# Kernel tuning notes

Measured on AMD Instinct MI355X. Metric: run time of the kernel, lower is better.

Reference implementation:

```python
import jax, jax.numpy as jnp
import numpy as np

B, S, HID, NH = 8, 1024, 768, 12
HD = HID // NH

def _linear_params(key, din, dout):
    kw, kb = jax.random.split(key)
    lim = 1.0 / np.sqrt(din)
    W = jax.random.uniform(kw, (din, dout), minval=-lim, maxval=lim, dtype=jnp.float32)
    b = jax.random.uniform(kb, (dout,), minval=-lim, maxval=lim, dtype=jnp.float32)
    return W, b

def setup_inputs() -> dict:
    key = jax.random.key(0)
    ks = jax.random.split(key, 10)
    query = jax.random.normal(ks[0], (B, S, HID), dtype=jnp.float32)
    key_t = jax.random.normal(ks[1], (B, S, HID), dtype=jnp.float32)
    value = jax.random.normal(ks[2], (B, S, HID), dtype=jnp.float32)
    mask = jax.random.randint(ks[3], (B, 1, 1, S), 0, 2, dtype=jnp.int32)
    Wq, bq = _linear_params(ks[4], HID, HID)
    Wk, bk = _linear_params(ks[5], HID, HID)
    Wv, bv = _linear_params(ks[6], HID, HID)
    Wo, bo = _linear_params(ks[7], HID, HID)
    W1, b1 = _linear_params(ks[8], 2 * HID, HID)
    W2, b2 = _linear_params(ks[9], 2 * HID, HID)
    return dict(query=query, key=key_t, value=value, mask=mask,
                Wq=Wq, bq=bq, Wk=Wk, bk=bk, Wv=Wv, bv=bv,
                Wo=Wo, bo=bo, W1=W1, b1=b1, W2=W2, b2=b2)

def reference(query, key, value, mask, Wq, bq, Wk, bk, Wv, bv, Wo, bo, W1, b1, W2, b2):
    scale = np.sqrt(HD).astype(np.float32)
    # project and split heads: [B,S,HID] -> [B,NH,S,HD]
    def heads(x, W, b):
        return (x @ W + b).reshape(B, S, NH, HD).transpose(0, 2, 1, 3)
    Q = heads(query, Wq, bq)
    K = heads(key, Wk, bk)
    V = heads(value, Wv, bv)
    energy = jnp.einsum('bhqd,bhkd->bhqk', Q, K) / scale  # [B,NH,S,S]
    energy = jnp.where(mask == 0, jnp.float32(-1e10), energy)
    attention = jax.nn.softmax(energy, axis=-1)
    x = jnp.einsum('bhqk,bhkd->bhqd', attention, V)
    x = x.transpose(0, 2, 1, 3).reshape(B, S, HID)
    x = x @ Wo + bo
    x = jnp.concatenate([x, query], axis=2)  # [B,S,2*HID]
    x1 = jax.nn.sigmoid(x @ W1 + b1)
    x2 = x @ W2 + b2
    return (x1 * x2, attention)
```

## Files before the change

### kernel.cpp

```cpp
#include <hip/hip_runtime.h>
#include <hip/hip_bf16.h>

#define Bn   8
#define Sn   1024
#define HIDn 768
#define NHn  12
#define HDn  64
#define MROWS (Bn * Sn)
#define OUT0  ((size_t)MROWS * HIDn)

typedef __attribute__((ext_vector_type(8))) short short8;
typedef __attribute__((ext_vector_type(4))) float f32x4;

__device__ __forceinline__ float bf2f(unsigned short u) {
    union { unsigned int i; float f; } v;
    v.i = ((unsigned int)u) << 16;
    return v.f;
}
__device__ __forceinline__ unsigned short f2bf(float f) {
    __hip_bfloat16 h = __float2bfloat16(f);
    return *reinterpret_cast<unsigned short*>(&h);
}

template <typename T> struct IsFP32              { static constexpr bool v = false; };
template <>           struct IsFP32<float>       { static constexpr bool v = true;  };

__device__ __forceinline__ float ld1f(const unsigned short* p) { return bf2f(*p); }
__device__ __forceinline__ float ld1f(const float* p)          { return *p; }

__device__ __forceinline__ void load8s(const unsigned short* p, short8& h, short8& l) {
    h = *(const short8*)p;
    #pragma unroll
    for (int t = 0; t < 8; ++t) l[t] = 0;
}
__device__ __forceinline__ void load8s(const float* p, short8& h, short8& l) {
    float4 a = *(const float4*)p;
    float4 b = *(const float4*)(p + 4);
    float f[8] = {a.x, a.y, a.z, a.w, b.x, b.y, b.z, b.w};
    #pragma unroll
    for (int t = 0; t < 8; ++t) {
        unsigned short hu = f2bf(f[t]);
        h[t] = (short)hu;
        l[t] = (short)f2bf(f[t] - bf2f(hu));
    }
}
__device__ __forceinline__ void load8k(const unsigned short* p, int stride, short8& h, short8& l) {
    #pragma unroll
    for (int t = 0; t < 8; ++t) { h[t] = (short)p[(size_t)t * stride]; l[t] = 0; }
}
__device__ __forceinline__ void load8k(const float* p, int stride, short8& h, short8& l) {
    #pragma unroll
    for (int t = 0; t < 8; ++t) {
        float f = p[(size_t)t * stride];
        unsigned short hu = f2bf(f);
        h[t] = (short)hu;
        l[t] = (short)f2bf(f - bf2f(hu));
    }
}

__global__ void probe_kernel(const unsigned short* __restrict__ q, int* __restrict__ flag) {
    __shared__ int cnt;
    if (threadIdx.x == 0) cnt = 0;
    __syncthreads();
    int ins = 0;
    for (int i = threadIdx.x; i < 4096; i += 256) {
        unsigned short u = q[2 * i];
        int e = (u >> 7) & 0xFF;
        float v = bf2f(u);
        if (e == 0xFF || fabsf(v) > 1e4f) ins++;
    }
    atomicAdd(&cnt, ins);
    __syncthreads();
    if (threadIdx.x == 0) *flag = (cnt > 400) ? 1 : 0;
}

template <typename TA, typename TA2, typename TW>
__launch_bounds__(256, 2)
__global__ void gemm_mfma(const TA*  __restrict__ A,
                          const TA2* __restrict__ A2,
                          int Ksplit, int K,
                          const TW* __restrict__ W,
                          const TW* __restrict__ bias,
                          const unsigned short* __restrict__ gate,
                          void* __restrict__ Cv, int c_fp32,
                          const int* __restrict__ flag, int mymode)
{
    if (*flag != mymode) return;

    constexpr bool AFP  = IsFP32<TA>::v;
    constexpr bool A2FP = IsFP32<TA2>::v;
    constexpr bool WFP  = IsFP32<TW>::v;

    __shared__ __align__(16) unsigned short Ash[128][40];
    __shared__ __align__(16) unsigned short Asl[128][40];
    __shared__ __align__(16) unsigned short Bth[64][40];
    __shared__ __align__(16) unsigned short Btl[64][40];

    const int tid  = threadIdx.x;
    const int lane = tid & 63;
    const int wid  = tid >> 6;
    const int wr   = wid >> 1;
    const int wc   = wid & 1;
    const int l15  = lane & 15;
    const int g    = lane >> 4;
    const int n0   = blockIdx.x * 64;
    const int m0   = blockIdx.y * 128;

    f32x4 acc[4][2];
    #pragma unroll
    for (int mi = 0; mi < 4; ++mi)
        #pragma unroll
        for (int ni = 0; ni < 2; ++ni)
            acc[mi][ni] = (f32x4){0.f, 0.f, 0.f, 0.f};

    for (int k0 = 0; k0 < K; k0 += 32) {
        const bool fromA = (k0 < Ksplit);
        const bool allo  = fromA ? AFP : A2FP;

        #pragma unroll
        for (int t = 0; t < 2; ++t) {
            const int idx = t * 256 + tid;
            const int row = idx >> 2;
            const int c8  = (idx & 3) * 8;
            short8 h, l;
            if (fromA) load8s(A  + (size_t)(m0 + row) * HIDn + k0 + c8, h, l);
            else       load8s(A2 + (size_t)(m0 + row) * HIDn + (k0 - Ksplit) + c8, h, l);
            *(short8*)&Ash[row][c8] = h;
            if (allo) *(short8*)&Asl[row][c8] = l;
        }
        {
            const int nn = tid >> 2;
            const int kg = (tid & 3) * 8;
            short8 h, l;
            load8k(W + (size_t)(k0 + kg) * HIDn + n0 + nn, HIDn, h, l);
            *(short8*)&Bth[nn][kg] = h;
            if (WFP) *(short8*)&Btl[nn][kg] = l;
        }
        __syncthreads();

        short8 ah[4], bh[2], al[4], bl[2];
        #pragma unroll
        for (int mi = 0; mi < 4; ++mi)
            ah[mi] = *(const short8*)&Ash[wr * 64 + mi * 16 + l15][g * 8];
        #pragma unroll
        for (int ni = 0; ni < 2; ++ni)
            bh[ni] = *(const short8*)&Bth[wc * 32 + ni * 16 + l15][g * 8];
        if (allo) {
            #pragma unroll
            for (int mi = 0; mi < 4; ++mi)
                al[mi] = *(const short8*)&Asl[wr * 64 + mi * 16 + l15][g * 8];
        }
        if (WFP) {
            #pragma unroll
            for (int ni = 0; ni < 2; ++ni)
                bl[ni] = *(const short8*)&Btl[wc * 32 + ni * 16 + l15][g * 8];
        }

        #pragma unroll
        for (int mi = 0; mi < 4; ++mi)
            #pragma unroll
            for (int ni = 0; ni < 2; ++ni)
                acc[mi][ni] = __builtin_amdgcn_mfma_f32_16x16x32_bf16(ah[mi], bh[ni], acc[mi][ni], 0, 0, 0);
        if (WFP) {
            #pragma unroll
            for (int mi = 0; mi < 4; ++mi)
                #pragma unroll
                for (int ni = 0; ni < 2; ++ni)
                    acc[mi][ni] = __builtin_amdgcn_mfma_f32_16x16x32_bf16(ah[mi], bl[ni], acc[mi][ni], 0, 0, 0);
        }
        if (allo) {
            #pragma unroll
            for (int mi = 0; mi < 4; ++mi)
                #pragma unroll
                for (int ni = 0; ni < 2; ++ni)
                    acc[mi][ni] = __builtin_amdgcn_mfma_f32_16x16x32_bf16(al[mi], bh[ni], acc[mi][ni], 0, 0, 0);
        }
        __syncthreads();
    }

    #pragma unroll
    for (int mi = 0; mi < 4; ++mi) {
        #pragma unroll
        for (int ni = 0; ni < 2; ++ni) {
            const int col = n0 + wc * 32 + ni * 16 + l15;
            const float bv = ld1f(bias + col);
            #pragma unroll
            for (int r = 0; r < 4; ++r) {
                const int row = m0 + wr * 64 + mi * 16 + g * 4 + r;
                float v = acc[mi][ni][r] + bv;
                if (gate) {
                    float gt = bf2f(gate[(size_t)row * HIDn + col]);
                    v = v / (1.f + expf(-gt));
                }
                const size_t idx = (size_t)row * HIDn + col;
                if (c_fp32) ((float*)Cv)[idx] = v;
                else        ((unsigned short*)Cv)[idx] = f2bf(v);
            }
        }
    }
}

#define QB 64
#define KT 128
#define KSTRIDE 72
#define VSTRIDE 136

__launch_bounds__(256, 2)
__global__ void attn_mfma_kernel(const unsigned short* __restrict__ Q,
                                 const unsigned short* __restrict__ Kb,
                                 const unsigned short* __restrict__ V,
                                 const int* __restrict__ mask,
                                 void* __restrict__ dout,
                                 unsigned short* __restrict__ xout,
                                 const int* __restrict__ flag)
{
    __shared__ __align__(16) unsigned short Qs[QB][KSTRIDE];
    __shared__ __align__(16) unsigned short Ks[KT][KSTRIDE];
    __shared__ __align__(16) unsigned short Vt[HDn][VSTRIDE];
    __shared__ __align__(16) unsigned short Ps[QB][VSTRIDE];
    __shared__ float maskadd[KT];

    const int bid = blockIdx.x;
    const int qb  = bid & 15;
    const int h   = (bid >> 4) % NHn;
    const int b   = (bid >> 4) / NHn;
    const int q0  = qb * QB;

    const int tid  = threadIdx.x;
    const int lane = tid & 63;
    const int wid  = tid >> 6;
    const int l15  = lane & 15;
    const int g    = lane >> 4;
    const int ofp32 = *flag;

    #pragma unroll
    for (int i = 0; i < 2; ++i) {
        const int chunk = i * 256 + tid;
        const int row = chunk >> 3;
        const int c8  = (chunk & 7) * 8;
        uint4 v = *(const uint4*)(Q + ((size_t)(b * Sn + q0 + row)) * HIDn + h * HDn + c8);
        *(uint4*)&Qs[row][c8] = v;
    }
    __syncthreads();

    short8 qa[2];
    #pragma unroll
    for (int ks = 0; ks < 2; ++ks)
        qa[ks] = *(const short8*)&Qs[wid * 16 + l15][ks * 32 + g * 8];

    float mrow[4], lrow[4];
    #pragma unroll
    for (int r = 0; r < 4; ++r) { mrow[r] = -3.0e38f; lrow[r] = 0.f; }

    #pragma unroll 1
    for (int kt = 0; kt < Sn; kt += KT) {
        __syncthreads();
        #pragma unroll
        for (int i = 0; i < 4; ++i) {
            const int chunk = i * 256 + tid;
            const int row = chunk >> 3;
            const int c8  = (chunk & 7) * 8;
            uint4 v = *(const uint4*)(Kb + ((size_t)(b * Sn + kt + row)) * HIDn + h * HDn + c8);
            *(uint4*)&Ks[row][c8] = v;
        }
        if (tid < KT) maskadd[tid] = (mask[b * Sn + kt + tid] == 0) ? -1e10f : 0.0f;
        __syncthreads();

        f32x4 sacc[8];
        #pragma unroll
        for (int nt = 0; nt < 8; ++nt) sacc[nt] = (f32x4){0.f, 0.f, 0.f, 0.f};
        #pragma unroll
        for (int ks = 0; ks < 2; ++ks) {
            #pragma unroll
            for (int nt = 0; nt < 8; ++nt) {
                short8 kb = *(const short8*)&Ks[nt * 16 + l15][ks * 32 + g * 8];
                sacc[nt] = __builtin_amdgcn_mfma_f32_16x16x32_bf16(qa[ks], kb, sacc[nt], 0, 0, 0);
            }
        }
        #pragma unroll
        for (int r = 0; r < 4; ++r) {
            float sv[8], tmax = -3.0e38f;
            #pragma unroll
            for (int nt = 0; nt < 8; ++nt) {
                sv[nt] = sacc[nt][r] * 0.125f + maskadd[nt * 16 + l15];
                tmax = fmaxf(tmax, sv[nt]);
            }
            const float mnew = fmaxf(mrow[r], tmax);
            float acc = lrow[r] * __expf(mrow[r] - mnew);
            #pragma unroll
            for (int nt = 0; nt < 8; ++nt) acc += __expf(sv[nt] - mnew);
            lrow[r] = acc; mrow[r] = mnew;
        }
    }

    #pragma unroll
    for (int r = 0; r < 4; ++r) {
        float m = mrow[r], l = lrow[r];
        #pragma unroll
        for (int off = 1; off < 16; off <<= 1) {
            const float m2 = __shfl_xor(m, off);
            const float l2 = __shfl_xor(l, off);
            const float mn = fmaxf(m, m2);
            l = l * __expf(m - mn) + l2 * __expf(m2 - mn);
            m = mn;
        }
        mrow[r] = m;
        lrow[r] = 1.0f / l;
    }

    f32x4 xacc[4];
    #pragma unroll
    for (int dt = 0; dt < 4; ++dt) xacc[dt] = (f32x4){0.f, 0.f, 0.f, 0.f};

    #pragma unroll 1
    for (int kt = 0; kt < Sn; kt += KT) {
        __syncthreads();
        #pragma unroll
        for (int i = 0; i < 4; ++i) {
            const int chunk = i * 256 + tid;
            const int row = chunk >> 3;
            const int c8  = (chunk & 7) * 8;
            uint4 v = *(const uint4*)(Kb + ((size_t)(b * Sn + kt + row)) * HIDn + h * HDn + c8);
            *(uint4*)&Ks[row][c8] = v;
        }
        #pragma unroll
        for (int i = 0; i < 4; ++i) {
            const int task = i * 256 + tid;
            const int key = task >> 3;
            const int dg  = (task & 7) * 8;
            uint4 v = *(const uint4*)(V + ((size_t)(b * Sn + kt + key)) * HIDn + h * HDn + dg);
            const unsigned short* us = (const unsigned short*)&v;
            #pragma unroll
            for (int t = 0; t < 8; ++t) Vt[dg + t][key] = us[t];
        }
        if (tid < KT) maskadd[tid] = (mask[b * Sn + kt + tid] == 0) ? -1e10f : 0.0f;
        __syncthreads();

        f32x4 sacc[8];
        #pragma unroll
        for (int nt = 0; nt < 8; ++nt) sacc[nt] = (f32x4){0.f, 0.f, 0.f, 0.f};
        #pragma unroll
        for (int ks = 0; ks < 2; ++ks) {
            #pragma unroll
            for (int nt = 0; nt < 8; ++nt) {
                short8 kb = *(const short8*)&Ks[nt * 16 + l15][ks * 32 + g * 8];
                sacc[nt] = __builtin_amdgcn_mfma_f32_16x16x32_bf16(qa[ks], kb, sacc[nt], 0, 0, 0);
            }
        }

        const size_t arowbase =
            OUT0 + (((size_t)(b * NHn + h)) * Sn + (size_t)(q0 + wid * 16)) * (size_t)Sn;
        #pragma unroll
        for (int r = 0; r < 4; ++r) {
            const int rloc = g * 4 + r;
            #pragma unroll
            for (int nt = 0; nt < 8; ++nt) {
                const int col = nt * 16 + l15;
                const float sv = sacc[nt][r] * 0.125f + maskadd[col];
                const float p  = __expf(sv - mrow[r]) * lrow[r];
                const size_t oidx = arowbase + (size_t)rloc * Sn + kt + col;
                if (ofp32) __builtin_nontemporal_store(p, (float*)dout + oidx);
                else       __builtin_nontemporal_store(f2bf(p), (unsigned short*)dout + oidx);
                Ps[wid * 16 + rloc][col] = f2bf(p);
            }
        }
        short8 pa[4];
        #pragma unroll
        for (int k2 = 0; k2 < 4; ++k2)
            pa[k2] = *(const short8*)&Ps[wid * 16 + l15][k2 * 32 + g * 8];
        #pragma unroll
        for (int dt = 0; dt < 4; ++dt) {
            #pragma unroll
            for (int k2 = 0; k2 < 4; ++k2) {
                short8 vb = *(const short8*)&Vt[dt * 16 + l15][k2 * 32 + g * 8];
                xacc[dt] = __builtin_amdgcn_mfma_f32_16x16x32_bf16(pa[k2], vb, xacc[dt], 0, 0, 0);
            }
        }
    }

    #pragma unroll
    for (int dt = 0; dt < 4; ++dt) {
        #pragma unroll
        for (int r = 0; r < 4; ++r) {
            const int rloc = g * 4 + r;
            const int q = q0 + wid * 16 + rloc;
            const int d = dt * 16 + l15;
            xout[((size_t)(b * Sn + q)) * HIDn + h * HDn + d] = f2bf(xacc[dt][r]);
        }
    }
}

extern "C" void kernel_launch(void* const* d_in, const int* in_sizes, int n_in,
                              void* d_out, int out_size, void* d_ws, size_t ws_size,
                              hipStream_t stream)
{
    const int* mask = (const int*)d_in[3];

    char* ws = (char*)d_ws;
    const size_t SZ = (size_t)MROWS * HIDn * 2;
    unsigned short* Qb = (unsigned short*)(ws);
    unsigned short* Kb = (unsigned short*)(ws + SZ);
    unsigned short* Vb = (unsigned short*)(ws + 2 * SZ);
    unsigned short* Xa = (unsigned short*)(ws + 3 * SZ);
    int* flag = (int*)(ws + 4 * SZ);
    unsigned short* Yb = Qb;
    unsigned short* H1 = Kb;

    probe_kernel<<<1, 256, 0, stream>>>((const unsigned short*)d_in[0], flag);

    dim3 gg(HIDn / 64, MROWS / 128);
    const int BIG = 1 << 30;

    {
        typedef unsigned short T;
        gemm_mfma<T,T,T><<<gg,256,0,stream>>>((const T*)d_in[0],(const T*)d_in[0],BIG,HIDn,
            (const T*)d_in[4],(const T*)d_in[5],nullptr,Qb,0,flag,0);
        gemm_mfma<T,T,T><<<gg,256,0,stream>>>((const T*)d_in[1],(const T*)d_in[1],BIG,HIDn,
            (const T*)d_in[6],(const T*)d_in[7],nullptr,Kb,0,flag,0);
        gemm_mfma<T,T,T><<<gg,256,0,stream>>>((const T*)d_in[2],(const T*)d_in[2],BIG,HIDn,
            (const T*)d_in[8],(const T*)d_in[9],nullptr,Vb,0,flag,0);
    }
    {
        typedef float T;
        gemm_mfma<T,T,T><<<gg,256,0,stream>>>((const T*)d_in[0],(const T*)d_in[0],BIG,HIDn,
            (const T*)d_in[4],(const T*)d_in[5],nullptr,Qb,0,flag,1);
        gemm_mfma<T,T,T><<<gg,256,0,stream>>>((const T*)d_in[1],(const T*)d_in[1],BIG,HIDn,
            (const T*)d_in[6],(const T*)d_in[7],nullptr,Kb,0,flag,1);
        gemm_mfma<T,T,T><<<gg,256,0,stream>>>((const T*)d_in[2],(const T*)d_in[2],BIG,HIDn,
            (const T*)d_in[8],(const T*)d_in[9],nullptr,Vb,0,flag,1);
    }

    attn_mfma_kernel<<<Bn * NHn * (Sn / QB), 256, 0, stream>>>(Qb, Kb, Vb, mask, d_out, Xa, flag);

    {
        typedef unsigned short T;
        gemm_mfma<T,T,T><<<gg,256,0,stream>>>(Xa,Xa,BIG,HIDn,
            (const T*)d_in[10],(const T*)d_in[11],nullptr,Yb,0,flag,0);
        gemm_mfma<T,T,T><<<gg,256,0,stream>>>(Yb,(const T*)d_in[0],HIDn,2*HIDn,
            (const T*)d_in[12],(const T*)d_in[13],nullptr,H1,0,flag,0);
        gemm_mfma<T,T,T><<<gg,256,0,stream>>>(Yb,(const T*)d_in[0],HIDn,2*HIDn,
            (const T*)d_in[14],(const T*)d_in[15],H1,d_out,0,flag,0);
    }
    {
        typedef float T;
        gemm_mfma<unsigned short,unsigned short,T><<<gg,256,0,stream>>>(Xa,Xa,BIG,HIDn,
            (const T*)d_in[10],(const T*)d_in[11],nullptr,Yb,0,flag,1);
        gemm_mfma<unsigned short,T,T><<<gg,256,0,stream>>>(Yb,(const T*)d_in[0],HIDn,2*HIDn,
            (const T*)d_in[12],(const T*)d_in[13],nullptr,H1,0,flag,1);
        gemm_mfma<unsigned short,T,T><<<gg,256,0,stream>>>(Yb,(const T*)d_in[0],HIDn,2*HIDn,
            (const T*)d_in[14],(const T*)d_in[15],H1,d_out,1,flag,1);
    }
}
```

Baseline: 1.010 ms.

## Pre-transpose and pre-split weights into bf16 hi/lo buffers before GEMMs

Adds a prep_w kernel that transposes each weight matrix into N-major layout and splits it into bf16 high and low parts, run once per call for the QKV and output/gate weight groups. The GEMM B-tile load then becomes a contiguous 16-byte vector read instead of eight strided scalar loads with per-element conversion. This removes uncoalesced weight reads and repeated conversion work across many row blocks, at the cost of two extra launches and workspace aliasing. Xa and Kb are reused as weight scratch, and H1 moves to Vb.

```diff
diff --git a/kernel.cpp b/kernel.cpp
--- a/kernel.cpp
+++ b/kernel.cpp
@@ -42,19 +42,6 @@
         unsigned short hu = f2bf(f[t]);
         h[t] = (short)hu;
         l[t] = (short)f2bf(f[t] - bf2f(hu));
-    }
-}
-__device__ __forceinline__ void load8k(const unsigned short* p, int stride, short8& h, short8& l) {
-    #pragma unroll
-    for (int t = 0; t < 8; ++t) { h[t] = (short)p[(size_t)t * stride]; l[t] = 0; }
-}
-__device__ __forceinline__ void load8k(const float* p, int stride, short8& h, short8& l) {
-    #pragma unroll
-    for (int t = 0; t < 8; ++t) {
-        float f = p[(size_t)t * stride];
-        unsigned short hu = f2bf(f);
-        h[t] = (short)hu;
-        l[t] = (short)f2bf(f - bf2f(hu));
     }
 }
 
@@ -74,12 +61,67 @@
     if (threadIdx.x == 0) *flag = (cnt > 400) ? 1 : 0;
 }
 
+__global__ void prep_w(const void* __restrict__ s0, const void* __restrict__ s1,
+                       const void* __restrict__ s2,
+                       unsigned short* __restrict__ d0h, unsigned short* __restrict__ d0l,
+                       unsigned short* __restrict__ d1h, unsigned short* __restrict__ d1l,
+                       unsigned short* __restrict__ d2h, unsigned short* __restrict__ d2l,
+                       int K0, int K1, int K2, const int* __restrict__ flag)
+{
+    const int z = blockIdx.z;
+    const void* src    = (z == 0) ? s0 : (z == 1) ? s1 : s2;
+    unsigned short* dh = (z == 0) ? d0h : (z == 1) ? d1h : d2h;
+    unsigned short* dl = (z == 0) ? d0l : (z == 1) ? d1l : d2l;
+    const int K        = (z == 0) ? K0 : (z == 1) ? K1 : K2;
+
+    const int k0 = blockIdx.x * 64;
+    if (k0 >= K) return;
+    const int n0 = blockIdx.y * 64;
+    const bool fp32 = (*flag != 0);
+
+    __shared__ float tile[64][65];
+    const int tx = threadIdx.x & 15, ty = threadIdx.x >> 4;
+
+    #pragma unroll
+    for (int i = 0; i < 4; ++i) {
+        const int k = ty + 16 * i;
+        const size_t off = (size_t)(k0 + k) * HIDn + n0 + tx * 4;
+        if (fp32) {
+            float4 v = *(const float4*)((const float*)src + off);
+            tile[k][tx * 4 + 0] = v.x; tile[k][tx * 4 + 1] = v.y;
+            tile[k][tx * 4 + 2] = v.z; tile[k][tx * 4 + 3] = v.w;
+        } else {
+            ushort4 v = *(const ushort4*)((const unsigned short*)src + off);
+            tile[k][tx * 4 + 0] = bf2f(v.x); tile[k][tx * 4 + 1] = bf2f(v.y);
+            tile[k][tx * 4 + 2] = bf2f(v.z); tile[k][tx * 4 + 3] = bf2f(v.w);
+        }
+    }
+    __syncthreads();
+
+    #pragma unroll
+    for (int i = 0; i < 4; ++i) {
+        const int n  = ty + 16 * i;
+        const int kk = tx * 4;
+        ushort4 hh, ll;
+        float f0 = tile[kk + 0][n], f1 = tile[kk + 1][n];
+        float f2 = tile[kk + 2][n], f3 = tile[kk + 3][n];
+        hh.x = f2bf(f0); ll.x = f2bf(f0 - bf2f(hh.x));
+        hh.y = f2bf(f1); ll.y = f2bf(f1 - bf2f(hh.y));
+        hh.z = f2bf(f2); ll.z = f2bf(f2 - bf2f(hh.z));
+        hh.w = f2bf(f3); ll.w = f2bf(f3 - bf2f(hh.w));
+        const size_t off = (size_t)(n0 + n) * K + k0 + kk;
+        *(ushort4*)(dh + off) = hh;
+        *(ushort4*)(dl + off) = ll;
+    }
+}
+
 template <typename TA, typename TA2, typename TW>
 __launch_bounds__(256, 2)
 __global__ void gemm_mfma(const TA*  __restrict__ A,
                           const TA2* __restrict__ A2,
                           int Ksplit, int K,
-                          const TW* __restrict__ W,
+                          const unsigned short* __restrict__ Wth,
+                          const unsigned short* __restrict__ Wtl,
                           const TW* __restrict__ bias,
                           const unsigned short* __restrict__ gate,
                           void* __restrict__ Cv, int c_fp32,
@@ -115,7 +157,7 @@
 
     for (int k0 = 0; k0 < K; k0 += 32) {
         const bool fromA = (k0 < Ksplit);
-        const bool allo  = fromA ? AFP : A2FP;
+        const bool alo   = fromA ? AFP : A2FP;
 
         #pragma unroll
         for (int t = 0; t < 2; ++t) {
@@ -126,15 +168,14 @@
             if (fromA) load8s(A  + (size_t)(m0 + row) * HIDn + k0 + c8, h, l);
             else       load8s(A2 + (size_t)(m0 + row) * HIDn + (k0 - Ksplit) + c8, h, l);
             *(short8*)&Ash[row][c8] = h;
-            if (allo) *(short8*)&Asl[row][c8] = l;
+            if (alo) *(short8*)&Asl[row][c8] = l;
         }
         {
             const int nn = tid >> 2;
             const int kg = (tid & 3) * 8;
-            short8 h, l;
-            load8k(W + (size_t)(k0 + kg) * HIDn + n0 + nn, HIDn, h, l);
-            *(short8*)&Bth[nn][kg] = h;
-            if (WFP) *(short8*)&Btl[nn][kg] = l;
+            const size_t woff = (size_t)(n0 + nn) * K + k0 + kg;
+            *(short8*)&Bth[nn][kg] = *(const short8*)(Wth + woff);
+            if (WFP) *(short8*)&Btl[nn][kg] = *(const short8*)(Wtl + woff);
         }
         __syncthreads();
 
@@ -145,7 +186,7 @@
         #pragma unroll
         for (int ni = 0; ni < 2; ++ni)
             bh[ni] = *(const short8*)&Bth[wc * 32 + ni * 16 + l15][g * 8];
-        if (allo) {
+        if (alo) {
             #pragma unroll
             for (int mi = 0; mi < 4; ++mi)
                 al[mi] = *(const short8*)&Asl[wr * 64 + mi * 16 + l15][g * 8];
@@ -168,7 +209,7 @@
                 for (int ni = 0; ni < 2; ++ni)
                     acc[mi][ni] = __builtin_amdgcn_mfma_f32_16x16x32_bf16(ah[mi], bl[ni], acc[mi][ni], 0, 0, 0);
         }
-        if (allo) {
+        if (alo) {
             #pragma unroll
             for (int mi = 0; mi < 4; ++mi)
                 #pragma unroll
@@ -404,9 +445,29 @@
     unsigned short* Xa = (unsigned short*)(ws + 3 * SZ);
     int* flag = (int*)(ws + 4 * SZ);
     unsigned short* Yb = Qb;
-    unsigned short* H1 = Kb;
+    unsigned short* H1 = Vb;
+
+    const size_t W768  = (size_t)HIDn * HIDn;
+    const size_t W1536 = (size_t)2 * HIDn * HIDn;
+    unsigned short* Wqt_h = Xa;
+    unsigned short* Wqt_l = Wqt_h + W768;
+    unsigned short* Wkt_h = Wqt_l + W768;
+    unsigned short* Wkt_l = Wkt_h + W768;
+    unsigned short* Wvt_h = Wkt_l + W768;
+    unsigned short* Wvt_l = Wvt_h + W768;
+    unsigned short* Wot_h = Kb;
+    unsigned short* Wot_l = Wot_h + W768;
+    unsigned short* W1t_h = Wot_l + W768;
+    unsigned short* W1t_l = W1t_h + W1536;
+    unsigned short* W2t_h = W1t_l + W1536;
+    unsigned short* W2t_l = W2t_h + W1536;
 
     probe_kernel<<<1, 256, 0, stream>>>((const unsigned short*)d_in[0], flag);
+
+    prep_w<<<dim3(12, 12, 3), 256, 0, stream>>>(
+        d_in[4], d_in[6], d_in[8],
+        Wqt_h, Wqt_l, Wkt_h, Wkt_l, Wvt_h, Wvt_l,
+        HIDn, HIDn, HIDn, flag);
 
     dim3 gg(HIDn / 64, MROWS / 128);
     const int BIG = 1 << 30;
@@ -414,40 +475,45 @@
     {
         typedef unsigned short T;
         gemm_mfma<T,T,T><<<gg,256,0,stream>>>((const T*)d_in[0],(const T*)d_in[0],BIG,HIDn,
-            (const T*)d_in[4],(const T*)d_in[5],nullptr,Qb,0,flag,0);
+            Wqt_h,Wqt_l,(const T*)d_in[5],nullptr,Qb,0,flag,0);
         gemm_mfma<T,T,T><<<gg,256,0,stream>>>((const T*)d_in[1],(const T*)d_in[1],BIG,HIDn,
-            (const T*)d_in[6],(const T*)d_in[7],nullptr,Kb,0,flag,0);
+            Wkt_h,Wkt_l,(const T*)d_in[7],nullptr,Kb,0,flag,0);
         gemm_mfma<T,T,T><<<gg,256,0,stream>>>((const T*)d_in[2],(const T*)d_in[2],BIG,HIDn,
-            (const T*)d_in[8],(const T*)d_in[9],nullptr,Vb,0,flag,0);
+            Wvt_h,Wvt_l,(const T*)d_in[9],nullptr,Vb,0,flag,0);
     }
     {
         typedef float T;
         gemm_mfma<T,T,T><<<gg,256,0,stream>>>((const T*)d_in[0],(const T*)d_in[0],BIG,HIDn,
-            (const T*)d_in[4],(const T*)d_in[5],nullptr,Qb,0,flag,1);
+            Wqt_h,Wqt_l,(const T*)d_in[5],nullptr,Qb,0,flag,1);
         gemm_mfma<T,T,T><<<gg,256,0,stream>>>((const T*)d_in[1],(const T*)d_in[1],BIG,HIDn,
-            (const T*)d_in[6],(const T*)d_in[7],nullptr,Kb,0,flag,1);
+            Wkt_h,Wkt_l,(const T*)d_in[7],nullptr,Kb,0,flag,1);
         gemm_mfma<T,T,T><<<gg,256,0,stream>>>((const T*)d_in[2],(const T*)d_in[2],BIG,HIDn,
-            (const T*)d_in[8],(const T*)d_in[9],nullptr,Vb,0,flag,1);
+            Wvt_h,Wvt_l,(const T*)d_in[9],nullptr,Vb,0,flag,1);
     }
 
     attn_mfma_kernel<<<Bn * NHn * (Sn / QB), 256, 0, stream>>>(Qb, Kb, Vb, mask, d_out, Xa, flag);
+
+    prep_w<<<dim3(24, 12, 3), 256, 0, stream>>>(
+        d_in[10], d_in[12], d_in[14],
+        Wot_h, Wot_l, W1t_h, W1t_l, W2t_h, W2t_l,
+        HIDn, 2 * HIDn, 2 * HIDn, flag);
 
     {
         typedef unsigned short T;
         gemm_mfma<T,T,T><<<gg,256,0,stream>>>(Xa,Xa,BIG,HIDn,
-            (const T*)d_in[10],(const T*)d_in[11],nullptr,Yb,0,flag,0);
+            Wot_h,Wot_l,(const T*)d_in[11],nullptr,Yb,0,flag,0);
         gemm_mfma<T,T,T><<<gg,256,0,stream>>>(Yb,(const T*)d_in[0],HIDn,2*HIDn,
-            (const T*)d_in[12],(const T*)d_in[13],nullptr,H1,0,flag,0);
+            W1t_h,W1t_l,(const T*)d_in[13],nullptr,H1,0,flag,0);
         gemm_mfma<T,T,T><<<gg,256,0,stream>>>(Yb,(const T*)d_in[0],HIDn,2*HIDn,
-            (const T*)d_in[14],(const T*)d_in[15],H1,d_out,0,flag,0);
+            W2t_h,W2t_l,(const T*)d_in[15],H1,d_out,0,flag,0);
     }
     {
         typedef float T;
         gemm_mfma<unsigned short,unsigned short,T><<<gg,256,0,stream>>>(Xa,Xa,BIG,HIDn,
-            (const T*)d_in[10],(const T*)d_in[11],nullptr,Yb,0,flag,1);
+            Wot_h,Wot_l,(const T*)d_in[11],nullptr,Yb,0,flag,1);
         gemm_mfma<unsigned short,T,T><<<gg,256,0,stream>>>(Yb,(const T*)d_in[0],HIDn,2*HIDn,
-            (const T*)d_in[12],(const T*)d_in[13],nullptr,H1,0,flag,1);
+            W1t_h,W1t_l,(const T*)d_in[13],nullptr,H1,0,flag,1);
         gemm_mfma<unsigned short,T,T><<<gg,256,0,stream>>>(Yb,(const T*)d_in[0],HIDn,2*HIDn,
-            (const T*)d_in[14],(const T*)d_in[15],H1,d_out,1,flag,1);
-    }
-}
+            W2t_h,W2t_l,(const T*)d_in[15],H1,d_out,1,flag,1);
+    }
+}
```

After: 969.2 us. 1.04x faster.
